# Performance work log

Hardware: AMD Instinct MI355X
Metric: run time of the kernel (lower is better)

The kernel has to match this reference:

```python
import jax, jax.numpy as jnp
import numpy as np

B, S, NB, ORDER, D = 256, 50, 8, 2, 128
N_ITEMS, N_RELS = 100000, 200
STDV = 1.0 / float(np.sqrt(D))  # reset_parameters: uniform(-1/sqrt(hidden), 1/sqrt(hidden))


def setup_inputs() -> dict:
    key = jax.random.key(0)
    ks = jax.random.split(key, 24)
    u = lambda k, shape: jax.random.uniform(k, shape, jnp.float32, -STDV, STDV)
    return {
        'h_iids': jax.random.randint(ks[0], (B, S), 1, N_ITEMS),
        'a_iids': jax.random.randint(ks[1], (B,), 0, N_ITEMS),
        'adj_entity': jax.random.randint(ks[2], (N_ITEMS, NB), 0, N_ITEMS),
        'adj_relation': jax.random.randint(ks[3], (N_ITEMS, NB), 0, N_RELS),
        'item_emb': u(ks[4], (N_ITEMS, D)),
        'rel_emb': u(ks[5], (N_RELS, D)),
        'Wa': u(ks[6], (D, 1)), 'ba': u(ks[7], (1,)),          # linear_attention
        'Wt': u(ks[8], (D, D)), 'bt': u(ks[9], (D,)),          # linear_attention_transform
        'Wih': u(ks[10], (D, 3 * D)), 'Whh': u(ks[11], (D, 3 * D)),  # GRU (1 layer)
        'bih': u(ks[12], (3 * D,)), 'bhh': u(ks[13], (3 * D,)),
        'W1': u(ks[14], (D, D)), 'b1': u(ks[15], (D,)),        # linear_one
        'W2': u(ks[16], (D, D)), 'b2': u(ks[17], (D,)),        # linear_two
        'W3': u(ks[18], (D, 1)),                               # linear_three (no bias)
        'Wtr': u(ks[19], (2 * D, D)), 'btr': u(ks[20], (D,)),  # linear_transform
    }


def _forward(h_iids, adj_entity, adj_relation, item_emb, rel_emb,
             Wa, ba, Wt, bt, Wih, Whh, bih, bhh,
             W1, b1, W2, b2, W3, Wtr, btr):
    # ---- get_neighbors: multi-hop KG neighbor expansion ----
    entities = [h_iids]           # level 0: [B, S]
    relations = []
    for i in range(ORDER):
        e = entities[i]
        entities.append(adj_entity[e].reshape(B, -1))    # [B, S*NB^(i+1)]
        relations.append(adj_relation[e].reshape(B, -1))
    ent_embs = [item_emb[e] for e in entities]           # gathers
    rel_embs = [rel_emb[r] for r in relations]
    # ---- high_order_aggregate: attention-weighted neighbor aggregation ----
    neib = ent_embs[ORDER]                                # [B, S*NB^ORDER, D]
    for i in range(ORDER):
        self_e = ent_embs[ORDER - i - 1]                  # [B, M, D]
        rel = rel_embs[ORDER - i - 1].reshape(B, -1, NB, D)
        nb4 = neib.reshape(rel.shape)                     # [B, M, NB, D]
        att = (self_e[:, :, None, :] * rel * nb4) @ Wa + ba   # [B, M, NB, 1]
        alpha = jax.nn.softmax(att, axis=2)
        agg = jnp.sum(nb4 * alpha, axis=2)                # [B, M, D]
        neib = (self_e + agg) @ Wt + bt                   # aggregate='sum' branch
    item_embs = neib                                      # [B, S, D] (sigmoid in src is dead code)
    # ---- GRU, 1 layer, batch_first ----
    def step(h, x):
        gi = x @ Wih + bih
        gh = h @ Whh + bhh
        ir, iz, inn = jnp.split(gi, 3, axis=-1)
        hr, hz, hn = jnp.split(gh, 3, axis=-1)
        r = jax.nn.sigmoid(ir + hr)
        z = jax.nn.sigmoid(iz + hz)
        n = jnp.tanh(inn + r * hn)
        h2 = (1.0 - z) * n + z * h
        return h2, h2
    h0 = jnp.zeros((B, D), jnp.float32)
    _, outs = jax.lax.scan(step, h0, jnp.swapaxes(item_embs, 0, 1))
    output = jnp.swapaxes(outs, 0, 1)                     # [B, S, D]
    # ---- attention pooling over sequence ----
    last_idx = jnp.clip(jnp.sum(h_iids != 0, axis=1) - 1, 0, S - 1)
    local_ht = output[jnp.arange(B), last_idx]            # [B, D]
    q1 = (local_ht @ W1 + b1)[:, None, :]
    q2 = output @ W2 + b2
    al = jax.nn.sigmoid(q1 + q2) @ W3                     # [B, S, 1]
    global_ht = jnp.sum(al * output, axis=1)
    ght = jnp.concatenate([local_ht, global_ht], axis=1) @ Wtr + btr
    logits = jax.nn.relu(ght @ item_emb.T)                # [B, n_items]
    return logits


def reference(h_iids, a_iids, adj_entity, adj_relation, item_emb, rel_emb,
              Wa, ba, Wt, bt, Wih, Whh, bih, bhh,
              W1, b1, W2, b2, W3, Wtr, btr):
    # a_iids is accepted by forward() but unused (matches the torch source).
    return _forward(h_iids, adj_entity, adj_relation, item_emb, rel_emb,
                    Wa, ba, Wt, bt, Wih, Whh, bih, bhh,
                    W1, b1, W2, b2, W3, Wtr, btr)
```

## Files before the change

kernel.cpp:

```cpp
#include <hip/hip_runtime.h>
#include <hip/hip_bf16.h>
#include <math.h>

#define NB_B 256
#define NB_S 50
#define NB_NB 8
#define NB_D 128
#define NB_NITEMS 100000

#define C_RZ (-1.442695041f)
#define C_N (2.885390082f)

typedef __attribute__((ext_vector_type(8))) short short8;
typedef __attribute__((ext_vector_type(4))) float f32x4;
typedef unsigned int uint;
typedef unsigned short ushort;

__device__ __forceinline__ ushort f2bf(float f) {
  union { float f; uint u; } v;
  v.f = f;
  return (ushort)((v.u + 0x7fffu + ((v.u >> 16) & 1u)) >> 16);
}
__device__ __forceinline__ uint packbf(float a, float b) {
  return (uint)f2bf(a) | ((uint)f2bf(b) << 16);
}
__device__ __forceinline__ float bflo(uint u) {
  union { uint u; float f; } v; v.u = u << 16; return v.f;
}
__device__ __forceinline__ float bfhi(uint u) {
  union { uint u; float f; } v; v.u = u & 0xffff0000u; return v.f;
}
__device__ __forceinline__ float bf2f(ushort u) {
  union { uint u; float f; } v; v.u = (uint)u << 16; return v.f;
}
__device__ __forceinline__ void unpack8(uint4 u, float* f) {
  f[0] = bflo(u.x); f[1] = bfhi(u.x);
  f[2] = bflo(u.y); f[3] = bfhi(u.y);
  f[4] = bflo(u.z); f[5] = bfhi(u.z);
  f[6] = bflo(u.w); f[7] = bfhi(u.w);
}

__device__ __forceinline__ void castf_body(const float* __restrict__ src,
                                           uint* __restrict__ dst, int i, int n8) {
  if (i >= n8) return;
  float4 a = ((const float4*)src)[2 * i];
  float4 b = ((const float4*)src)[2 * i + 1];
  uint4 o;
  o.x = packbf(a.x, a.y);
  o.y = packbf(a.z, a.w);
  o.z = packbf(b.x, b.y);
  o.w = packbf(b.z, b.w);
  ((uint4*)dst)[i] = o;
}
template <int CO, bool SCALED>
__device__ __forceinline__ void castT_body(const float* __restrict__ W,
                                           ushort* __restrict__ WT, int idx) {
  if (idx >= 128 * CO) return;
  int n = idx >> 7, k = idx & 127;
  float v = W[(size_t)k * CO + n];
  if (SCALED) v *= (n < 256 ? C_RZ : C_N);
  WT[idx] = f2bf(v);
}
__global__ __launch_bounds__(256) void prep_kernel(
    const float* __restrict__ item_emb, const float* __restrict__ rel_emb,
    const float* __restrict__ Wt, const float* __restrict__ Wih,
    const float* __restrict__ Whh, const float* __restrict__ W2,
    const float* __restrict__ bih, const float* __restrict__ bhh,
    uint* __restrict__ EMB_BF, uint* __restrict__ REL_BF,
    ushort* __restrict__ WtT, ushort* __restrict__ WihT,
    ushort* __restrict__ WhhT, ushort* __restrict__ W2T,
    float* __restrict__ GIBIAS) {
  int bx = blockIdx.x, tid = threadIdx.x;
  if (bx < 6250) {
    castf_body(item_emb, EMB_BF, bx * 256 + tid, 1600000);
  } else if (bx < 6263) {
    castf_body(rel_emb, REL_BF, (bx - 6250) * 256 + tid, 3200);
  } else if (bx < 6327) {
    castT_body<128, false>(Wt, WtT, (bx - 6263) * 256 + tid);
  } else if (bx < 6519) {
    castT_body<384, true>(Wih, WihT, (bx - 6327) * 256 + tid);
  } else if (bx < 6711) {
    castT_body<384, true>(Whh, WhhT, (bx - 6519) * 256 + tid);
  } else if (bx < 6775) {
    castT_body<128, false>(W2, W2T, (bx - 6711) * 256 + tid);
  } else {
    int idx = (bx - 6775) * 256 + tid;
    if (idx < 384) {
      float s = (idx < 256) ? C_RZ : C_N;
      GIBIAS[idx] = s * bih[idx] + (idx < 256 ? s * bhh[idx] : 0.f);
    }
  }
}

__device__ __forceinline__ uint4 hop_pair4(
    int e_self, int q, int p, const int* __restrict__ adj_e,
    const int* __restrict__ adj_r, const uint* __restrict__ embB,
    const uint* __restrict__ relB, const uint* __restrict__ neibB,
    const float* __restrict__ Wa, float* __restrict__ alds) {
  uint4 us = ((const uint4*)(embB + (size_t)e_self * 64))[q];
  float s[8], wa[8], sw[8];
  unpack8(us, s);
  *(float4*)&wa[0] = ((const float4*)Wa)[q * 2];
  *(float4*)&wa[4] = ((const float4*)Wa)[q * 2 + 1];
#pragma unroll
  for (int d = 0; d < 8; d++) sw[d] = s[d] * wa[d];

  int4 ra = ((const int4*)(adj_r + (size_t)e_self * 8))[0];
  int4 rb = ((const int4*)(adj_r + (size_t)e_self * 8))[1];
  int rk[8] = {ra.x, ra.y, ra.z, ra.w, rb.x, rb.y, rb.z, rb.w};

  uint4 nbp[8];
  if (neibB == nullptr) {
    int4 ea = ((const int4*)(adj_e + (size_t)e_self * 8))[0];
    int4 eb = ((const int4*)(adj_e + (size_t)e_self * 8))[1];
    int e2[8] = {ea.x, ea.y, ea.z, ea.w, eb.x, eb.y, eb.z, eb.w};
#pragma unroll
    for (int k = 0; k < 8; k++)
      nbp[k] = ((const uint4*)(embB + (size_t)e2[k] * 64))[q];
  } else {
#pragma unroll
    for (int k = 0; k < 8; k++)
      nbp[k] = ((const uint4*)(neibB + ((size_t)p * 8 + k) * 64))[q];
  }

  float t[8];
#pragma unroll
  for (int k = 0; k < 8; k++) {
    uint4 ur = ((const uint4*)(relB + (size_t)rk[k] * 64))[q];
    float rr[8], nb[8];
    unpack8(ur, rr);
    unpack8(nbp[k], nb);
    float tt = 0.f;
#pragma unroll
    for (int d = 0; d < 8; d++) tt = fmaf(sw[d] * rr[d], nb[d], tt);
    t[k] = tt;
  }

  bool b0 = (q & 1), b1 = (q & 2), b2 = (q & 4);
  float a4[4];
#pragma unroll
  for (int i = 0; i < 4; i++) {
    float send = b0 ? t[i] : t[4 + i];
    float recv = __shfl_xor(send, 1);
    a4[i] = (b0 ? t[4 + i] : t[i]) + recv;
  }
  float a2[2];
#pragma unroll
  for (int i = 0; i < 2; i++) {
    float send = b1 ? a4[i] : a4[2 + i];
    float recv = __shfl_xor(send, 2);
    a2[i] = (b1 ? a4[2 + i] : a4[i]) + recv;
  }
  float send1 = b2 ? a2[0] : a2[1];
  float recv1 = __shfl_xor(send1, 4);
  float c = (b2 ? a2[1] : a2[0]) + recv1;
  c += __shfl_xor(c, 8);

  float e = __expf(c);
  float den = e;
  den += __shfl_xor(den, 1);
  den += __shfl_xor(den, 2);
  den += __shfl_xor(den, 4);
  float alpha = e * __builtin_amdgcn_rcpf(den);

  int kstar = (q & 1) * 4 + (q & 2) + ((q & 4) >> 2);
  if (q < 8) alds[kstar] = alpha;
  asm volatile("s_waitcnt lgkmcnt(0)" ::: "memory");
  float a8[8];
  *(float4*)&a8[0] = ((const float4*)alds)[0];
  *(float4*)&a8[4] = ((const float4*)alds)[1];

  float x[8];
#pragma unroll
  for (int d = 0; d < 8; d++) x[d] = s[d];
#pragma unroll
  for (int k = 0; k < 8; k++) {
    float nb[8];
    unpack8(nbp[k], nb);
#pragma unroll
    for (int d = 0; d < 8; d++) x[d] = fmaf(a8[k], nb[d], x[d]);
  }
  uint4 o;
  o.x = packbf(x[0], x[1]);
  o.y = packbf(x[2], x[3]);
  o.z = packbf(x[4], x[5]);
  o.w = packbf(x[6], x[7]);
  return o;
}

__global__ __launch_bounds__(256) void hoplin_kernel(
    const int* __restrict__ h_iids, const int* __restrict__ adj_e,
    const int* __restrict__ adj_r, const uint* __restrict__ embB,
    const uint* __restrict__ relB, const float* __restrict__ Wa,
    const ushort* __restrict__ WtT, const float* __restrict__ bt,
    ushort* __restrict__ NEIB) {
  __shared__ ushort X0s[16 * 128];
  __shared__ float als[16][8];
  const int bx = blockIdx.x;
  const int wv = threadIdx.x >> 6, ln = threadIdx.x & 63;
  const int g = ln >> 4, q = ln & 15;
  const int lp = wv * 4 + g;
  const int p = bx * 16 + lp;

  int b = p / (NB_S * NB_NB);
  int m = p % (NB_S * NB_NB);
  int h = h_iids[b * NB_S + (m >> 3)];
  int e_self = adj_e[h * NB_NB + (m & 7)];
  uint4 o = hop_pair4(e_self, q, p, adj_e, adj_r, embB, relB, nullptr, Wa,
                      als[lp]);
  {
    int byte = (lp * 256 + q * 16) ^ ((lp & 7) << 4);
    *(uint4*)((char*)X0s + byte) = o;
  }
  __syncthreads();

  const int lr = ln & 15, lg = ln >> 4;
  short8 afr[4];
#pragma unroll
  for (int kf = 0; kf < 4; kf++) {
    int byte = (lr * 256 + lg * 16 + kf * 64) ^ ((lr & 7) << 4);
    afr[kf] = *(const short8*)((const char*)X0s + byte);
  }
  f32x4 acc[2] = {};
#pragma unroll
  for (int nf = 0; nf < 2; nf++) {
    int n = (wv * 2 + nf) * 16 + lr;
    const ushort* bb = WtT + (size_t)n * 128 + lg * 8;
#pragma unroll
    for (int kf = 0; kf < 4; kf++) {
      short8 bv = *(const short8*)(bb + kf * 32);
      acc[nf] = __builtin_amdgcn_mfma_f32_16x16x32_bf16(afr[kf], bv, acc[nf],
                                                        0, 0, 0);
    }
  }
#pragma unroll
  for (int nf = 0; nf < 2; nf++) {
    int n = (wv * 2 + nf) * 16 + lr;
    float bv = bt[n];
#pragma unroll
    for (int r = 0; r < 4; r++) {
      int mg = bx * 16 + lg * 4 + r;
      NEIB[(size_t)mg * 128 + n] = f2bf(acc[nf][r] + bv);
    }
  }
}

__global__ __launch_bounds__(256) void hopgi_kernel(
    const int* __restrict__ h_iids, const int* __restrict__ adj_e,
    const int* __restrict__ adj_r, const uint* __restrict__ embB,
    const uint* __restrict__ relB, const uint* __restrict__ neibB,
    const float* __restrict__ Wa, const ushort* __restrict__ WtT,
    const float* __restrict__ bt, const ushort* __restrict__ WihT,
    const float* __restrict__ GIBIAS, float* __restrict__ GI) {
  __shared__ ushort X1s[16 * 128];
  __shared__ ushort SEQs[16 * 128];
  __shared__ float als[16][8];
  const int wv = threadIdx.x >> 6, ln = threadIdx.x & 63;
  const int g = ln >> 4, q = ln & 15;
  const int lp = wv * 4 + g;
  const int p = blockIdx.x * 16 + lp;

  int e_self = h_iids[p];
  uint4 o = hop_pair4(e_self, q, p, adj_e, adj_r, embB, relB, neibB, Wa, als[lp]);
  {
    int byte = (lp * 256 + q * 16) ^ ((lp & 7) << 4);
    *(uint4*)((char*)X1s + byte) = o;
  }
  __syncthreads();

  const int lr = ln & 15, lg = ln >> 4;
  {
    short8 afr[4];
#pragma unroll
    for (int kf = 0; kf < 4; kf++) {
      int byte = (lr * 256 + lg * 16 + kf * 64) ^ ((lr & 7) << 4);
      afr[kf] = *(const short8*)((const char*)X1s + byte);
    }
    f32x4 acc[2] = {};
#pragma unroll
    for (int nf = 0; nf < 2; nf++) {
      int n = (wv * 2 + nf) * 16 + lr;
      const ushort* bb = WtT + (size_t)n * 128 + lg * 8;
#pragma unroll
      for (int kf = 0; kf < 4; kf++) {
        short8 b = *(const short8*)(bb + kf * 32);
        acc[nf] = __builtin_amdgcn_mfma_f32_16x16x32_bf16(afr[kf], b, acc[nf],
                                                          0, 0, 0);
      }
    }
#pragma unroll
    for (int nf = 0; nf < 2; nf++) {
      int n = (wv * 2 + nf) * 16 + lr;
      float bv = bt[n];
#pragma unroll
      for (int r = 0; r < 4; r++) {
        int m = lg * 4 + r;
        int byte = (m * 256 + n * 2) ^ ((m & 7) << 4);
        *(ushort*)((char*)SEQs + byte) = f2bf(acc[nf][r] + bv);
      }
    }
  }
  __syncthreads();

  {
    short8 sfr[4];
#pragma unroll
    for (int kf = 0; kf < 4; kf++) {
      int byte = (lr * 256 + lg * 16 + kf * 64) ^ ((lr & 7) << 4);
      sfr[kf] = *(const short8*)((const char*)SEQs + byte);
    }
#pragma unroll
    for (int i = 0; i < 6; i++) {
      int n = (wv * 6 + i) * 16 + lr;
      const ushort* bb = WihT + (size_t)n * 128 + lg * 8;
      f32x4 a2 = {};
#pragma unroll
      for (int kf = 0; kf < 4; kf++) {
        short8 b = *(const short8*)(bb + kf * 32);
        a2 = __builtin_amdgcn_mfma_f32_16x16x32_bf16(sfr[kf], b, a2, 0, 0, 0);
      }
      float bv = GIBIAS[n];
#pragma unroll
      for (int r = 0; r < 4; r++) {
        int m = lg * 4 + r;
        GI[(size_t)(blockIdx.x * 16 + m) * 384 + n] = a2[r] + bv;
      }
    }
  }
}

__global__ __launch_bounds__(512) void gru_mfma_kernel(
    const float* __restrict__ GI, const ushort* __restrict__ WhhT_bf,
    const float* __restrict__ bhh, ushort* __restrict__ OUTB) {
  const int b0 = blockIdx.x * 16;
  const int tid = threadIdx.x;
  const int w = tid >> 6, ln = tid & 63;
  const int lr = ln & 15, lg = ln >> 4;
  const int j = w * 16 + lr;

  __shared__ ushort hA[16 * 128];
  __shared__ ushort hB[16 * 128];

  short8 bfr[3][4];
#pragma unroll
  for (int g = 0; g < 3; g++) {
    const ushort* bb = WhhT_bf + (size_t)(g * 128 + j) * 128 + lg * 8;
#pragma unroll
    for (int kf = 0; kf < 4; kf++) bfr[g][kf] = *(const short8*)(bb + kf * 32);
  }
  const float bhn = C_N * bhh[256 + j];

  float h_reg[4] = {0.f, 0.f, 0.f, 0.f};

  {
    uint* hz = (uint*)hA;
#pragma unroll
    for (int i = tid; i < 1024; i += 512) hz[i] = 0;
  }
  __syncthreads();

  float girA[4][3], girB[4][3], girC[4][3], girD[4][3];
#pragma unroll
  for (int r = 0; r < 4; r++) {
    const float* g0 = GI + ((size_t)(b0 + lg * 4 + r) * NB_S + 0) * 384 + j;
    girA[r][0] = g0[0]; girA[r][1] = g0[128]; girA[r][2] = g0[256];
    const float* g1 = GI + ((size_t)(b0 + lg * 4 + r) * NB_S + 1) * 384 + j;
    girB[r][0] = g1[0]; girB[r][1] = g1[128]; girB[r][2] = g1[256];
    const float* g2 = GI + ((size_t)(b0 + lg * 4 + r) * NB_S + 2) * 384 + j;
    girC[r][0] = g2[0]; girC[r][1] = g2[128]; girC[r][2] = g2[256];
  }

  auto STEP = [&](int t, ushort* hRead, ushort* hWrite, float (&cur)[4][3],
                  float (&pre3)[4][3]) {
    if (t + 3 < NB_S) {
#pragma unroll
      for (int r = 0; r < 4; r++) {
        const float* g = GI + ((size_t)(b0 + lg * 4 + r) * NB_S + (t + 3)) * 384 + j;
        pre3[r][0] = g[0]; pre3[r][1] = g[128]; pre3[r][2] = g[256];
      }
    }
    __builtin_amdgcn_sched_barrier(0);
    short8 afr[4];
#pragma unroll
    for (int kf = 0; kf < 4; kf++) {
      int byte = (lr * 256 + kf * 64 + lg * 16) ^ ((lr & 7) << 4);
      afr[kf] = *(const short8*)((const char*)hRead + byte);
    }
    f32x4 acc[3] = {};
#pragma unroll
    for (int g = 0; g < 3; g++)
#pragma unroll
      for (int kf = 0; kf < 4; kf++)
        acc[g] = __builtin_amdgcn_mfma_f32_16x16x32_bf16(afr[kf], bfr[g][kf],
                                                         acc[g], 0, 0, 0);
#pragma unroll
    for (int r = 0; r < 4; r++) {
      int b = lg * 4 + r;
      float rg = __builtin_amdgcn_rcpf(
          1.f + __builtin_amdgcn_exp2f(cur[r][0] + acc[0][r]));
      float ze = __builtin_amdgcn_exp2f(cur[r][1] + acc[1][r]);
      float xp = cur[r][2] + rg * (bhn + acc[2][r]);
      float e2 = __builtin_amdgcn_exp2f(xp);
      float n = 1.f - 2.f * __builtin_amdgcn_rcpf(e2 + 1.f);
      float h2 = n + (h_reg[r] - n) * __builtin_amdgcn_rcpf(1.f + ze);
      h_reg[r] = h2;
      ushort hb = f2bf(h2);
      OUTB[((size_t)(b0 + b) * NB_S + t) * 128 + j] = hb;
      int byte = (b * 256 + j * 2) ^ ((b & 7) << 4);
      *(ushort*)((char*)hWrite + byte) = hb;
    }
    asm volatile("s_waitcnt lgkmcnt(0)" ::: "memory");
    __builtin_amdgcn_s_barrier();
  };

  for (int g4 = 0; g4 < 12; g4++) {
    int t = g4 * 4;
    STEP(t + 0, hA, hB, girA, girD);
    STEP(t + 1, hB, hA, girB, girA);
    STEP(t + 2, hA, hB, girC, girB);
    STEP(t + 3, hB, hA, girD, girC);
  }
  STEP(48, hA, hB, girA, girD);
  STEP(49, hB, hA, girB, girA);
}

__global__ __launch_bounds__(256) void pool_kernel(
    const int* __restrict__ h_iids, const ushort* __restrict__ OUTB,
    const float* __restrict__ W1, const float* __restrict__ b1,
    const ushort* __restrict__ W2T, const float* __restrict__ b2,
    const float* __restrict__ W3, const float* __restrict__ Wtr,
    const float* __restrict__ btr, ushort* __restrict__ GHT_bf) {
  const int b = blockIdx.x, tid = threadIdx.x;
  __shared__ float lh[128];
  __shared__ float q1[128];
  __shared__ float al[64];
  __shared__ float cat[256];

  if (tid < 128) {
    int cnt = 0;
    for (int s = 0; s < NB_S; s++) cnt += (h_iids[b * NB_S + s] != 0);
    int li = min(max(cnt - 1, 0), NB_S - 1);
    lh[tid] = bf2f(OUTB[((size_t)b * NB_S + li) * 128 + tid]);
  }
  __syncthreads();
  if (tid < 128) {
    float acc = b1[tid];
    for (int d = 0; d < 128; d++) acc += lh[d] * W1[(size_t)d * 128 + tid];
    q1[tid] = acc;
  }
  __syncthreads();

  {
    const int wv = tid >> 6, ln = tid & 63, lr = ln & 15, lg = ln >> 4;
    const int s0 = wv * 16;
    short8 zz = {0, 0, 0, 0, 0, 0, 0, 0};
    short8 afr[4];
    int srow = s0 + lr;
#pragma unroll
    for (int kf = 0; kf < 4; kf++)
      afr[kf] = (srow < NB_S)
                    ? *(const short8*)(OUTB + ((size_t)b * NB_S + srow) * 128 +
                                       lg * 8 + kf * 32)
                    : zz;
    float part[4] = {0.f, 0.f, 0.f, 0.f};
#pragma unroll
    for (int nf = 0; nf < 8; nf++) {
      const ushort* bb = W2T + (size_t)(nf * 16 + lr) * 128 + lg * 8;
      f32x4 acc = {};
#pragma unroll
      for (int kf = 0; kf < 4; kf++) {
        short8 bv = *(const short8*)(bb + kf * 32);
        acc = __builtin_amdgcn_mfma_f32_16x16x32_bf16(afr[kf], bv, acc, 0, 0, 0);
      }
      int c = nf * 16 + lr;
      float qc = q1[c] + b2[c];
      float w3 = W3[c];
#pragma unroll
      for (int r = 0; r < 4; r++)
        part[r] += w3 / (1.f + __expf(-(qc + acc[r])));
    }
#pragma unroll
    for (int r = 0; r < 4; r++) {
#pragma unroll
      for (int off = 1; off < 16; off <<= 1) part[r] += __shfl_xor(part[r], off);
      int s = s0 + lg * 4 + r;
      if (lr == 0 && s < NB_S) al[s] = part[r];
    }
  }
  __syncthreads();

  if (tid < 128) {
    float g = 0.f;
    for (int s = 0; s < NB_S; s++)
      g += al[s] * bf2f(OUTB[((size_t)b * NB_S + s) * 128 + tid]);
    cat[tid] = lh[tid];
    cat[128 + tid] = g;
  }
  __syncthreads();
  if (tid < 128) {
    float acc = btr[tid];
    for (int dd = 0; dd < 256; dd++) acc += cat[dd] * Wtr[(size_t)dd * 128 + tid];
    GHT_bf[b * 128 + tid] = f2bf(acc);
  }
}

__global__ __launch_bounds__(256) void logits_mfma_kernel(
    const ushort* __restrict__ GHT_bf, const ushort* __restrict__ embB,
    float* __restrict__ out) {
  int wave = (int)(blockIdx.x * 4 + (threadIdx.x >> 6));
  int ln = threadIdx.x & 63;
  int n0 = __builtin_amdgcn_readfirstlane(wave) * 32;
  if (n0 >= NB_NITEMS) return;
  int lr = ln & 15, lg = ln >> 4;

  short8 bfr[2][4];
#pragma unroll
  for (int nf = 0; nf < 2; nf++) {
    const ushort* base = embB + (size_t)(n0 + nf * 16 + lr) * 128 + lg * 8;
#pragma unroll
    for (int kf = 0; kf < 4; kf++) bfr[nf][kf] = *(const short8*)(base + kf * 32);
  }

  f32x4 acc[16][2] = {};
#pragma unroll
  for (int mg = 0; mg < 4; mg++) {
    short8 afr[4][4];
#pragma unroll
    for (int mf = 0; mf < 4; mf++) {
      const ushort* ab = GHT_bf + (size_t)((mg * 4 + mf) * 16 + lr) * 128 + lg * 8;
#pragma unroll
      for (int kf = 0; kf < 4; kf++) afr[mf][kf] = *(const short8*)(ab + kf * 32);
    }
#pragma unroll
    for (int mf = 0; mf < 4; mf++)
#pragma unroll
      for (int nf = 0; nf < 2; nf++)
#pragma unroll
        for (int kf = 0; kf < 4; kf++)
          acc[mg * 4 + mf][nf] = __builtin_amdgcn_mfma_f32_16x16x32_bf16(
              afr[mf][kf], bfr[nf][kf], acc[mg * 4 + mf][nf], 0, 0, 0);
  }

#pragma unroll
  for (int mf = 0; mf < 16; mf++)
#pragma unroll
    for (int nf = 0; nf < 2; nf++) {
      int n = n0 + nf * 16 + lr;
#pragma unroll
      for (int r = 0; r < 4; r++) {
        int m = mf * 16 + lg * 4 + r;
        out[(size_t)m * NB_NITEMS + n] = fmaxf(acc[mf][nf][r], 0.f);
      }
    }
}

extern "C" void kernel_launch(void* const* d_in, const int* in_sizes, int n_in,
                              void* d_out, int out_size, void* d_ws, size_t ws_size,
                              hipStream_t stream) {
  const int* h_iids = (const int*)d_in[0];
  const int* adj_e = (const int*)d_in[2];
  const int* adj_r = (const int*)d_in[3];
  const float* item_emb = (const float*)d_in[4];
  const float* rel_emb = (const float*)d_in[5];
  const float* Wa = (const float*)d_in[6];
  const float* Wt = (const float*)d_in[8];
  const float* bt = (const float*)d_in[9];
  const float* Wih = (const float*)d_in[10];
  const float* Whh = (const float*)d_in[11];
  const float* bih = (const float*)d_in[12];
  const float* bhh = (const float*)d_in[13];
  const float* W1 = (const float*)d_in[14];
  const float* b1 = (const float*)d_in[15];
  const float* W2 = (const float*)d_in[16];
  const float* b2 = (const float*)d_in[17];
  const float* W3 = (const float*)d_in[18];
  const float* Wtr = (const float*)d_in[19];
  const float* btr = (const float*)d_in[20];
  float* out = (float*)d_out;

  char* w = (char*)d_ws;
  uint* EMB_BF = (uint*)w;                    w += 25600000;
  uint* REL_BF = (uint*)w;                    w += 51200;
  ushort* WtT_bf = (ushort*)w;                w += 32768;
  ushort* WihT_bf = (ushort*)w;               w += 98304;
  ushort* WhhT_bf = (ushort*)w;               w += 98304;
  ushort* W2T_bf = (ushort*)w;                w += 32768;
  float* GIBIAS = (float*)w;                  w += 2048;
  uint* NEIB_bf = (uint*)w;                   w += 26214400;
  float* GI = (float*)w;                      w += 19660800;
  ushort* OUTB = (ushort*)w;                  w += 3276800;
  ushort* GHT_bf = (ushort*)w;                w += 65536;

  prep_kernel<<<6777, 256, 0, stream>>>(item_emb, rel_emb, Wt, Wih, Whh, W2,
                                        bih, bhh, EMB_BF, REL_BF, WtT_bf,
                                        WihT_bf, WhhT_bf, W2T_bf, GIBIAS);

  hoplin_kernel<<<6400, 256, 0, stream>>>(h_iids, adj_e, adj_r, EMB_BF, REL_BF,
                                          Wa, WtT_bf, bt, (ushort*)NEIB_bf);
  hopgi_kernel<<<800, 256, 0, stream>>>(h_iids, adj_e, adj_r, EMB_BF, REL_BF,
                                        NEIB_bf, Wa, WtT_bf, bt, WihT_bf,
                                        GIBIAS, GI);

  gru_mfma_kernel<<<16, 512, 0, stream>>>(GI, WhhT_bf, bhh, OUTB);
  pool_kernel<<<256, 256, 0, stream>>>(h_iids, OUTB, W1, b1, W2T_bf, b2, W3,
                                       Wtr, btr, GHT_bf);

  logits_mfma_kernel<<<782, 256, 0, stream>>>(GHT_bf, (const ushort*)EMB_BF, out);
}
```

Before: 213.9 us.

## Retile logits GEMM per block and precompute first-hop entity ids in prep

The logits kernel is retiled so each block handles 128 items and each wave handles 64 batch rows. A-fragments (GHT) are loaded once per wave while item embeddings stream through per 16-column fragment, which cuts register pressure from 32 accumulators of 16x16 to 4x8. The out-of-bounds tail is handled by clamping loads and masking stores. Separately, the prep kernel now precomputes the first-hop neighbor ids into a workspace array E0, so hoplin no longer does the division and dependent double gather; this adds 400 extra prep blocks and one more indirection buffer.

```diff
diff --git a/kernel.cpp b/kernel.cpp
--- a/kernel.cpp
+++ b/kernel.cpp
@@ -66,10 +66,11 @@
     const float* __restrict__ Wt, const float* __restrict__ Wih,
     const float* __restrict__ Whh, const float* __restrict__ W2,
     const float* __restrict__ bih, const float* __restrict__ bhh,
+    const int* __restrict__ h_iids, const int* __restrict__ adj_e,
     uint* __restrict__ EMB_BF, uint* __restrict__ REL_BF,
     ushort* __restrict__ WtT, ushort* __restrict__ WihT,
     ushort* __restrict__ WhhT, ushort* __restrict__ W2T,
-    float* __restrict__ GIBIAS) {
+    float* __restrict__ GIBIAS, int* __restrict__ E0) {
   int bx = blockIdx.x, tid = threadIdx.x;
   if (bx < 6250) {
     castf_body(item_emb, EMB_BF, bx * 256 + tid, 1600000);
@@ -83,11 +84,21 @@
     castT_body<384, true>(Whh, WhhT, (bx - 6519) * 256 + tid);
   } else if (bx < 6775) {
     castT_body<128, false>(W2, W2T, (bx - 6711) * 256 + tid);
+  } else if (bx < 6776) {
+    int idx = tid;
+    if (idx < 256) {
+      GIBIAS[idx] = C_RZ * (bih[idx] + bhh[idx]);
+    }
+  } else if (bx < 6777) {
+    int idx = 256 + tid;
+    if (idx < 384) GIBIAS[idx] = C_N * bih[idx];
   } else {
-    int idx = (bx - 6775) * 256 + tid;
-    if (idx < 384) {
-      float s = (idx < 256) ? C_RZ : C_N;
-      GIBIAS[idx] = s * bih[idx] + (idx < 256 ? s * bhh[idx] : 0.f);
+    int p = (bx - 6777) * 256 + tid;
+    if (p < NB_B * NB_S * NB_NB) {
+      int b = p / (NB_S * NB_NB);
+      int m = p % (NB_S * NB_NB);
+      int h = h_iids[b * NB_S + (m >> 3)];
+      E0[p] = adj_e[h * NB_NB + (m & 7)];
     }
   }
 }
@@ -189,7 +200,7 @@
 }
 
 __global__ __launch_bounds__(256) void hoplin_kernel(
-    const int* __restrict__ h_iids, const int* __restrict__ adj_e,
+    const int* __restrict__ E0, const int* __restrict__ adj_e,
     const int* __restrict__ adj_r, const uint* __restrict__ embB,
     const uint* __restrict__ relB, const float* __restrict__ Wa,
     const ushort* __restrict__ WtT, const float* __restrict__ bt,
@@ -202,10 +213,7 @@
   const int lp = wv * 4 + g;
   const int p = bx * 16 + lp;
 
-  int b = p / (NB_S * NB_NB);
-  int m = p % (NB_S * NB_NB);
-  int h = h_iids[b * NB_S + (m >> 3)];
-  int e_self = adj_e[h * NB_NB + (m & 7)];
+  int e_self = E0[p];
   uint4 o = hop_pair4(e_self, q, p, adj_e, adj_r, embB, relB, nullptr, Wa,
                       als[lp]);
   {
@@ -507,49 +515,46 @@
 __global__ __launch_bounds__(256) void logits_mfma_kernel(
     const ushort* __restrict__ GHT_bf, const ushort* __restrict__ embB,
     float* __restrict__ out) {
-  int wave = (int)(blockIdx.x * 4 + (threadIdx.x >> 6));
-  int ln = threadIdx.x & 63;
-  int n0 = __builtin_amdgcn_readfirstlane(wave) * 32;
-  if (n0 >= NB_NITEMS) return;
-  int lr = ln & 15, lg = ln >> 4;
-
-  short8 bfr[2][4];
-#pragma unroll
-  for (int nf = 0; nf < 2; nf++) {
-    const ushort* base = embB + (size_t)(n0 + nf * 16 + lr) * 128 + lg * 8;
-#pragma unroll
-    for (int kf = 0; kf < 4; kf++) bfr[nf][kf] = *(const short8*)(base + kf * 32);
-  }
-
-  f32x4 acc[16][2] = {};
-#pragma unroll
-  for (int mg = 0; mg < 4; mg++) {
-    short8 afr[4][4];
-#pragma unroll
-    for (int mf = 0; mf < 4; mf++) {
-      const ushort* ab = GHT_bf + (size_t)((mg * 4 + mf) * 16 + lr) * 128 + lg * 8;
-#pragma unroll
-      for (int kf = 0; kf < 4; kf++) afr[mf][kf] = *(const short8*)(ab + kf * 32);
-    }
+  const int wv = threadIdx.x >> 6, ln = threadIdx.x & 63;
+  const int lr = ln & 15, lg = ln >> 4;
+  const int n0 = blockIdx.x * 128;
+  const int m0 = wv * 64;
+
+  short8 afr[4][4];
+#pragma unroll
+  for (int mf = 0; mf < 4; mf++) {
+    const ushort* ab = GHT_bf + (size_t)(m0 + mf * 16 + lr) * 128 + lg * 8;
+#pragma unroll
+    for (int kf = 0; kf < 4; kf++) afr[mf][kf] = *(const short8*)(ab + kf * 32);
+  }
+
+  f32x4 acc[4][8] = {};
+#pragma unroll
+  for (int nf = 0; nf < 8; nf++) {
+    int n = n0 + nf * 16 + lr;
+    int nc = min(n, NB_NITEMS - 1);
+    const ushort* bb = embB + (size_t)nc * 128 + lg * 8;
+    short8 b0_[4];
+#pragma unroll
+    for (int kf = 0; kf < 4; kf++) b0_[kf] = *(const short8*)(bb + kf * 32);
 #pragma unroll
     for (int mf = 0; mf < 4; mf++)
 #pragma unroll
-      for (int nf = 0; nf < 2; nf++)
-#pragma unroll
-        for (int kf = 0; kf < 4; kf++)
-          acc[mg * 4 + mf][nf] = __builtin_amdgcn_mfma_f32_16x16x32_bf16(
-              afr[mf][kf], bfr[nf][kf], acc[mg * 4 + mf][nf], 0, 0, 0);
-  }
-
-#pragma unroll
-  for (int mf = 0; mf < 16; mf++)
-#pragma unroll
-    for (int nf = 0; nf < 2; nf++) {
-      int n = n0 + nf * 16 + lr;
-#pragma unroll
-      for (int r = 0; r < 4; r++) {
-        int m = mf * 16 + lg * 4 + r;
-        out[(size_t)m * NB_NITEMS + n] = fmaxf(acc[mf][nf][r], 0.f);
+      for (int kf = 0; kf < 4; kf++)
+        acc[mf][nf] = __builtin_amdgcn_mfma_f32_16x16x32_bf16(
+            afr[mf][kf], b0_[kf], acc[mf][nf], 0, 0, 0);
+  }
+
+#pragma unroll
+  for (int mf = 0; mf < 4; mf++)
+#pragma unroll
+    for (int r = 0; r < 4; r++) {
+      int m = m0 + mf * 16 + lg * 4 + r;
+#pragma unroll
+      for (int nf = 0; nf < 8; nf++) {
+        int n = n0 + nf * 16 + lr;
+        if (n < NB_NITEMS)
+          out[(size_t)m * NB_NITEMS + n] = fmaxf(acc[mf][nf][r], 0.f);
       }
     }
 }
@@ -586,16 +591,18 @@
   ushort* WhhT_bf = (ushort*)w;               w += 98304;
   ushort* W2T_bf = (ushort*)w;                w += 32768;
   float* GIBIAS = (float*)w;                  w += 2048;
+  int* E0 = (int*)w;                          w += 409600;
   uint* NEIB_bf = (uint*)w;                   w += 26214400;
   float* GI = (float*)w;                      w += 19660800;
   ushort* OUTB = (ushort*)w;                  w += 3276800;
   ushort* GHT_bf = (ushort*)w;                w += 65536;
 
-  prep_kernel<<<6777, 256, 0, stream>>>(item_emb, rel_emb, Wt, Wih, Whh, W2,
-                                        bih, bhh, EMB_BF, REL_BF, WtT_bf,
-                                        WihT_bf, WhhT_bf, W2T_bf, GIBIAS);
-
-  hoplin_kernel<<<6400, 256, 0, stream>>>(h_iids, adj_e, adj_r, EMB_BF, REL_BF,
+  prep_kernel<<<7177, 256, 0, stream>>>(item_emb, rel_emb, Wt, Wih, Whh, W2,
+                                        bih, bhh, h_iids, adj_e, EMB_BF, REL_BF,
+                                        WtT_bf, WihT_bf, WhhT_bf, W2T_bf,
+                                        GIBIAS, E0);
+
+  hoplin_kernel<<<6400, 256, 0, stream>>>(E0, adj_e, adj_r, EMB_BF, REL_BF,
                                           Wa, WtT_bf, bt, (ushort*)NEIB_bf);
   hopgi_kernel<<<800, 256, 0, stream>>>(h_iids, adj_e, adj_r, EMB_BF, REL_BF,
                                         NEIB_bf, Wa, WtT_bf, bt, WihT_bf,
```

Measured after the change: 191.0 us (median of 2 runs). -10.7%, faster.
